# Optimization experiments

Measured on AMD Instinct MI355X. Metric: run time of the kernel, lower is better.

## Reference

```python
import jax, jax.numpy as jnp
import numpy as np
from jax import lax

B, C, H, W = 8, 1, 256, 256
BIG = float(H + W)  # larger than any possible in-image distance


def _dist_1d_along_h(feat):
    # feat: bool (B,H,W). Exact 1D distance along axis 1 to nearest True pixel.
    def step(d, f):
        d = jnp.where(f, 0.0, d + 1.0)
        return d, d

    init = jnp.full((feat.shape[0], feat.shape[2]), BIG, dtype=jnp.float32)
    ft = jnp.moveaxis(feat, 1, 0)  # (H,B,W)
    _, fwd = lax.scan(step, init, ft)
    _, bwd = lax.scan(step, init, ft[::-1])
    g = jnp.minimum(fwd, bwd[::-1])  # (H,B,W)
    return jnp.moveaxis(g, 0, 1)  # (B,H,W)


def _edt(feat):
    # Exact 2D Euclidean distance transform to nearest True pixel.
    # Decomposition: D2(i,j) = min_{j'} ( g(i,j')^2 + (j-j')^2 ),
    # where g is the exact 1D vertical distance within each column.
    g = jnp.minimum(_dist_1d_along_h(feat), BIG)
    g2 = g * g  # (B,H,W')
    j = jnp.arange(feat.shape[2], dtype=jnp.float32)
    offs = (j[:, None] - j[None, :]) ** 2  # (W, W')
    d2 = jnp.min(g2[:, :, None, :] + offs[None, None, :, :], axis=-1)  # (B,H,W)
    return jnp.sqrt(d2)


def _level_set(targets):
    # Faithful port of compute_level_set_function.
    m = targets[:, 0] != 0  # (B,H,W) foreground
    # scipy.distance_transform_edt(mask): distance of nonzero pixels to nearest zero -> features = background
    dist_inside = _edt(~m)
    # distance_transform_edt(1-mask): features = foreground
    dist_outside = _edt(m)
    phi = dist_outside - dist_inside
    denom = jnp.max(jnp.abs(phi), axis=(1, 2), keepdims=True) + 1e-8
    phi = phi / denom
    has_fg = jnp.any(m, axis=(1, 2), keepdims=True)
    phi = jnp.where(has_fg, phi, 0.0)  # empty-mask short-circuit -> zeros
    return phi[:, None].astype(jnp.float32)  # (B,1,H,W)


def setup_inputs() -> dict:
    key = jax.random.key(0)
    k1, k2 = jax.random.split(key)
    predictions = jax.random.normal(k1, (B, C, H, W), dtype=jnp.float32)
    targets = jax.random.randint(k2, (B, C, H, W), 0, 2, dtype=jnp.int32)
    return {"predictions": predictions, "targets": targets}


def reference(predictions, targets):
    probs = jax.nn.sigmoid(predictions)
    phi_G = _level_set(targets)
    return jnp.mean(phi_G * probs)
```

## Files before the change

### kernel.cpp

```cpp
#include <hip/hip_runtime.h>
#include <math.h>

#define BB 8
#define HH 256
#define WW 256
#define NPIX (BB*HH*WW)
#define NROWS (BB*HH)


__global__ void colscan(const int* __restrict__ tgt,
                        float2* __restrict__ g2) {
    int tx = threadIdx.x;
    int s = tx & 31, c = tx >> 5;
    int bw = blockIdx.x;
    int b = bw >> 4;
    int w = ((bw & 15) << 4) + c;
    const int* col = tgt + b * (HH * WW) + w;
    int base = s << 3;

    unsigned fgbits = 0;
    #pragma unroll
    for (int r = 0; r < 8; ++r)
        fgbits |= (col[(base + r) * WW] != 0 ? 1u : 0u) << r;
    unsigned bgbits = (~fgbits) & 0xFFu;

    const int BIGI = 1 << 20;
    int hiF = fgbits ? base + (31 - __clz(fgbits)) : -1;
    int hiB = bgbits ? base + (31 - __clz(bgbits)) : -1;
    int loF = fgbits ? base + (__ffs(fgbits) - 1) : BIGI;
    int loB = bgbits ? base + (__ffs(bgbits) - 1) : BIGI;

    int aF = hiF, aB = hiB;
    #pragma unroll
    for (int d = 1; d < 32; d <<= 1) {
        int vF = __shfl_up(aF, d, 32);
        int vB = __shfl_up(aB, d, 32);
        if (s >= d) { aF = max(aF, vF); aB = max(aB, vB); }
    }
    int pF = __shfl_up(aF, 1, 32);
    int pB = __shfl_up(aB, 1, 32);
    if (s == 0) { pF = -1; pB = -1; }
    if (pF < 0) pF = -BIGI;
    if (pB < 0) pB = -BIGI;

    int cF = loF, cB = loB;
    #pragma unroll
    for (int d = 1; d < 32; d <<= 1) {
        int vF = __shfl_down(cF, d, 32);
        int vB = __shfl_down(cB, d, 32);
        if (s < 32 - d) { cF = min(cF, vF); cB = min(cB, vB); }
    }
    int nF = __shfl_down(cF, 1, 32);
    int nB = __shfl_down(cB, 1, 32);
    if (s == 31) { nF = BIGI; nB = BIGI; }

    int dDF[8], dDB[8];
    int dF = nF - (base + 8);
    int dB = nB - (base + 8);
    #pragma unroll
    for (int r = 7; r >= 0; --r) {
        dF = ((fgbits >> r) & 1) ? 0 : dF + 1;
        dB = ((bgbits >> r) & 1) ? 0 : dB + 1;
        dDF[r] = dF; dDB[r] = dB;
    }

    float2* out = g2 + b * (HH * WW) + w;
    int uF = (base - 1) - pF;
    int uB = (base - 1) - pB;
    #pragma unroll
    for (int r = 0; r < 8; ++r) {
        uF = ((fgbits >> r) & 1) ? 0 : uF + 1;
        uB = ((bgbits >> r) & 1) ? 0 : uB + 1;
        int gF = min(min(uF, dDF[r]), 512);
        int gB = min(min(uB, dDB[r]), 512);
        float fB = (float)gB, fF = (float)gF;
        float2 o; o.x = fB * fB; o.y = fF * fF;
        out[(base + r) * WW] = o;
    }
}

__global__ void edt_fuse(const float2* __restrict__ g2,
                         const float* __restrict__ pred,
                         float* __restrict__ part_max,
                         double* __restrict__ part_sum,
                         int* __restrict__ part_fg) {
    __shared__ float sB[3 * WW];
    __shared__ float sF[3 * WW];
    __shared__ float wmax[4];
    __shared__ double wsum[4];
    __shared__ int wfg[4];
    int row = blockIdx.x;
    int j = threadIdx.x;

    float x = pred[row * WW + j];
    float2 v = g2[row * WW + j];
    sB[j] = 1e30f; sB[2 * WW + j] = 1e30f; sB[WW + j] = v.x;
    sF[j] = 1e30f; sF[2 * WW + j] = 1e30f; sF[WW + j] = v.y;
    bool isBg = (v.x == 0.0f);
    unsigned long long fgb = __ballot(v.y == 0.0f);
    __syncthreads();

    const float* sp = isBg ? sF : sB;
    float m = isBg ? v.y : v.x;
    int idx = WW + j;
    for (int k = 1; k < WW; ++k) {
        float k2 = (float)(k * k);
        if (k2 >= m) break;
        m = fminf(m, sp[idx - k] + k2);
        m = fminf(m, sp[idx + k] + k2);
    }
    float dist = sqrtf(m);
    float phi = isBg ? dist : -dist;
    float prob = 1.0f / (1.0f + expf(-x));
    double sd = (double)(phi * prob);
    float mx = dist;

    #pragma unroll
    for (int off = 32; off; off >>= 1) {
        mx = fmaxf(mx, __shfl_down(mx, off));
        sd += __shfl_down(sd, off);
    }
    int wid = j >> 6;
    if ((j & 63) == 0) { wmax[wid] = mx; wsum[wid] = sd; wfg[wid] = (fgb != 0ull); }
    __syncthreads();
    if (j == 0) {
        part_max[row] = fmaxf(fmaxf(wmax[0], wmax[1]), fmaxf(wmax[2], wmax[3]));
        part_sum[row] = wsum[0] + wsum[1] + wsum[2] + wsum[3];
        part_fg[row] = wfg[0] | wfg[1] | wfg[2] | wfg[3];
    }
}

__global__ void reduce_out(const float* __restrict__ part_max,
                           const double* __restrict__ part_sum,
                           const int* __restrict__ part_fg,
                           float* __restrict__ out) {
    __shared__ double terms[8];
    int tx = threadIdx.x;
    int wv = tx >> 6, l = tx & 63;
    #pragma unroll
    for (int q = 0; q < 2; ++q) {
        int b = wv * 2 + q;
        int base = b * HH;
        float mx = fmaxf(fmaxf(part_max[base + l], part_max[base + l + 64]),
                         fmaxf(part_max[base + l + 128], part_max[base + l + 192]));
        double sd = part_sum[base + l] + part_sum[base + l + 64]
                  + part_sum[base + l + 128] + part_sum[base + l + 192];
        int fg = part_fg[base + l] | part_fg[base + l + 64]
               | part_fg[base + l + 128] | part_fg[base + l + 192];
        #pragma unroll
        for (int off = 32; off; off >>= 1) {
            mx = fmaxf(mx, __shfl_down(mx, off));
            sd += __shfl_down(sd, off);
            fg |= __shfl_down(fg, off);
        }
        if (l == 0) terms[b] = fg ? sd / ((double)mx + 1e-8) : 0.0;
    }
    __syncthreads();
    if (tx == 0) {
        double t = 0.0;
        #pragma unroll
        for (int b = 0; b < BB; ++b) t += terms[b];
        out[0] = (float)(t / (double)NPIX);
    }
}

extern "C" void kernel_launch(void* const* d_in, const int* in_sizes, int n_in,
                              void* d_out, int out_size, void* d_ws, size_t ws_size,
                              hipStream_t stream) {
    const float* pred = (const float*)d_in[0];
    const int* tgt = (const int*)d_in[1];
    float* out = (float*)d_out;

    char* ws = (char*)d_ws;
    float* part_max = (float*)ws;
    double* part_sum = (double*)(ws + 8192);
    int* part_fg = (int*)(ws + 24576);
    float2* g2 = (float2*)(ws + 65536);

    colscan<<<128, 512, 0, stream>>>(tgt, g2);
    edt_fuse<<<NROWS, WW, 0, stream>>>(g2, pred, part_max, part_sum, part_fg);
    reduce_out<<<1, 256, 0, stream>>>(part_max, part_sum, part_fg, out);
}
```

Measured before the change: 67.15 us.

## Replace column-scan float2 buffer with bit-packed mask and per-row recompute

```diff
diff --git a/kernel.cpp b/kernel.cpp
--- a/kernel.cpp
+++ b/kernel.cpp
@@ -8,100 +8,72 @@
 #define NROWS (BB*HH)
 
 
-__global__ void colscan(const int* __restrict__ tgt,
-                        float2* __restrict__ g2) {
-    int tx = threadIdx.x;
-    int s = tx & 31, c = tx >> 5;
-    int bw = blockIdx.x;
-    int b = bw >> 4;
-    int w = ((bw & 15) << 4) + c;
-    const int* col = tgt + b * (HH * WW) + w;
-    int base = s << 3;
-
-    unsigned fgbits = 0;
+__global__ void maskbuild(const int* __restrict__ tgt,
+                          unsigned* __restrict__ fg_words) {
+    int blk = blockIdx.x;
+    int b = blk >> 3, band = blk & 7;
+    int j = threadIdx.x;
+    const int* base = tgt + b * (HH * WW) + (band * 32) * WW + j;
+    unsigned bits = 0;
     #pragma unroll
-    for (int r = 0; r < 8; ++r)
-        fgbits |= (col[(base + r) * WW] != 0 ? 1u : 0u) << r;
-    unsigned bgbits = (~fgbits) & 0xFFu;
-
-    const int BIGI = 1 << 20;
-    int hiF = fgbits ? base + (31 - __clz(fgbits)) : -1;
-    int hiB = bgbits ? base + (31 - __clz(bgbits)) : -1;
-    int loF = fgbits ? base + (__ffs(fgbits) - 1) : BIGI;
-    int loB = bgbits ? base + (__ffs(bgbits) - 1) : BIGI;
-
-    int aF = hiF, aB = hiB;
-    #pragma unroll
-    for (int d = 1; d < 32; d <<= 1) {
-        int vF = __shfl_up(aF, d, 32);
-        int vB = __shfl_up(aB, d, 32);
-        if (s >= d) { aF = max(aF, vF); aB = max(aB, vB); }
-    }
-    int pF = __shfl_up(aF, 1, 32);
-    int pB = __shfl_up(aB, 1, 32);
-    if (s == 0) { pF = -1; pB = -1; }
-    if (pF < 0) pF = -BIGI;
-    if (pB < 0) pB = -BIGI;
-
-    int cF = loF, cB = loB;
-    #pragma unroll
-    for (int d = 1; d < 32; d <<= 1) {
-        int vF = __shfl_down(cF, d, 32);
-        int vB = __shfl_down(cB, d, 32);
-        if (s < 32 - d) { cF = min(cF, vF); cB = min(cB, vB); }
-    }
-    int nF = __shfl_down(cF, 1, 32);
-    int nB = __shfl_down(cB, 1, 32);
-    if (s == 31) { nF = BIGI; nB = BIGI; }
-
-    int dDF[8], dDB[8];
-    int dF = nF - (base + 8);
-    int dB = nB - (base + 8);
-    #pragma unroll
-    for (int r = 7; r >= 0; --r) {
-        dF = ((fgbits >> r) & 1) ? 0 : dF + 1;
-        dB = ((bgbits >> r) & 1) ? 0 : dB + 1;
-        dDF[r] = dF; dDB[r] = dB;
-    }
-
-    float2* out = g2 + b * (HH * WW) + w;
-    int uF = (base - 1) - pF;
-    int uB = (base - 1) - pB;
-    #pragma unroll
-    for (int r = 0; r < 8; ++r) {
-        uF = ((fgbits >> r) & 1) ? 0 : uF + 1;
-        uB = ((bgbits >> r) & 1) ? 0 : uB + 1;
-        int gF = min(min(uF, dDF[r]), 512);
-        int gB = min(min(uB, dDB[r]), 512);
-        float fB = (float)gB, fF = (float)gF;
-        float2 o; o.x = fB * fB; o.y = fF * fF;
-        out[(base + r) * WW] = o;
-    }
+    for (int r = 0; r < 32; ++r)
+        bits |= (base[r * WW] != 0 ? 1u : 0u) << r;
+    fg_words[b * 2048 + band * 256 + j] = bits;
 }
 
-__global__ void edt_fuse(const float2* __restrict__ g2,
-                         const float* __restrict__ pred,
-                         float* __restrict__ part_max,
-                         double* __restrict__ part_sum,
-                         int* __restrict__ part_fg) {
+__global__ void edt_row(const unsigned* __restrict__ fg_words,
+                        const float* __restrict__ pred,
+                        float* __restrict__ part_max,
+                        double* __restrict__ part_sum,
+                        int* __restrict__ part_fg) {
+    __shared__ unsigned maskL[256 * 9];
     __shared__ float sB[3 * WW];
     __shared__ float sF[3 * WW];
     __shared__ float wmax[4];
     __shared__ double wsum[4];
     __shared__ int wfg[4];
+
     int row = blockIdx.x;
+    int b = row >> 8, i = row & 255;
     int j = threadIdx.x;
 
     float x = pred[row * WW + j];
-    float2 v = g2[row * WW + j];
-    sB[j] = 1e30f; sB[2 * WW + j] = 1e30f; sB[WW + j] = v.x;
-    sF[j] = 1e30f; sF[2 * WW + j] = 1e30f; sF[WW + j] = v.y;
-    bool isBg = (v.x == 0.0f);
-    unsigned long long fgb = __ballot(v.y == 0.0f);
+
+    const unsigned* mb = fg_words + b * 2048;
+    #pragma unroll
+    for (int w = 0; w < 8; ++w)
+        maskL[j * 9 + w] = mb[w * 256 + j];
     __syncthreads();
 
-    const float* sp = isBg ? sF : sB;
-    float m = isBg ? v.y : v.x;
+    const int BIGI = 1 << 20;
+    int pF = -BIGI, pB = -BIGI, nF = BIGI, nB = BIGI;
+    #pragma unroll
+    for (int w = 0; w < 4; ++w) {
+        unsigned long long v = (unsigned long long)maskL[j * 9 + 2 * w]
+                             | ((unsigned long long)maskL[j * 9 + 2 * w + 1] << 32);
+        unsigned long long g = ~v;
+        int d = i - 64 * w;
+        unsigned long long bf = (d >= 63) ? v : ((d < 0) ? 0ull : (v & (~0ull >> (63 - d))));
+        unsigned long long bb = (d >= 63) ? g : ((d < 0) ? 0ull : (g & (~0ull >> (63 - d))));
+        if (bf) pF = 64 * w + 63 - __builtin_clzll(bf);
+        if (bb) pB = 64 * w + 63 - __builtin_clzll(bb);
+        unsigned long long af = (d <= 0) ? v : ((d > 63) ? 0ull : (v & (~0ull << d)));
+        unsigned long long ab = (d <= 0) ? g : ((d > 63) ? 0ull : (g & (~0ull << d)));
+        if (af) nF = min(nF, 64 * w + __builtin_ctzll(af));
+        if (ab) nB = min(nB, 64 * w + __builtin_ctzll(ab));
+    }
+    int gF = min(min(i - pF, nF - i), 512);
+    int gB = min(min(i - pB, nB - i), 512);
+    bool isFg = (gF == 0);
+    unsigned long long fgb = __ballot(isFg);
+
+    float fF = (float)gF, fB = (float)gB;
+    sF[j] = 1e30f; sF[2 * WW + j] = 1e30f; sF[WW + j] = fF * fF;
+    sB[j] = 1e30f; sB[2 * WW + j] = 1e30f; sB[WW + j] = fB * fB;
+    __syncthreads();
+
+    const float* sp = isFg ? sB : sF;
+    float m = isFg ? fB * fB : fF * fF;
     int idx = WW + j;
     for (int k = 1; k < WW; ++k) {
         float k2 = (float)(k * k);
@@ -110,7 +82,7 @@
         m = fminf(m, sp[idx + k] + k2);
     }
     float dist = sqrtf(m);
-    float phi = isBg ? dist : -dist;
+    float phi = isFg ? -dist : dist;
     float prob = 1.0f / (1.0f + expf(-x));
     double sd = (double)(phi * prob);
     float mx = dist;
@@ -175,9 +147,9 @@
     float* part_max = (float*)ws;
     double* part_sum = (double*)(ws + 8192);
     int* part_fg = (int*)(ws + 24576);
-    float2* g2 = (float2*)(ws + 65536);
+    unsigned* fg_words = (unsigned*)(ws + 32768);
 
-    colscan<<<128, 512, 0, stream>>>(tgt, g2);
-    edt_fuse<<<NROWS, WW, 0, stream>>>(g2, pred, part_max, part_sum, part_fg);
+    maskbuild<<<64, 256, 0, stream>>>(tgt, fg_words);
+    edt_row<<<NROWS, WW, 0, stream>>>(fg_words, pred, part_max, part_sum, part_fg);
     reduce_out<<<1, 256, 0, stream>>>(part_max, part_sum, part_fg, out);
 }
```

Result: faster. 64.38 us (-4.1%).
